# Kernel optimization log

Hardware: AMD Instinct MI355X
Metric: run time of the kernel (lower is better)

The kernel has to match this reference:

```python
import jax, jax.numpy as jnp
import numpy as np

NF = 64
UP = 4
# ktype 's' tap offsets within the 3x3 window
TAPS = ((0, 0), (0, 1), (1, 0), (1, 1))


def setup_inputs() -> dict:
    key = jax.random.key(0)
    ks = jax.random.split(key, 14)
    B, C, H, W = 8, 3, 192, 192
    x = jax.random.normal(ks[0], (B, C, H, W), dtype=jnp.float32)
    def lin(k, fan_in, fan_out):
        s = 1.0 / np.sqrt(fan_in)
        return jax.random.uniform(k, (fan_out, fan_in), jnp.float32, -s, s)
    def bias(k, fan_in, fan_out):
        s = 1.0 / np.sqrt(fan_in)
        return jax.random.uniform(k, (fan_out,), jnp.float32, -s, s)
    inp = {"x": x}
    inp["W1"], inp["b1"] = lin(ks[1], 4, NF), bias(ks[2], 4, NF)
    inp["W2"], inp["b2"] = lin(ks[3], NF, NF), bias(ks[4], NF, NF)
    inp["W3"], inp["b3"] = lin(ks[5], NF, NF), bias(ks[6], NF, NF)
    inp["W4"], inp["b4"] = lin(ks[7], NF, NF), bias(ks[8], NF, NF)
    inp["W5"], inp["b5"] = lin(ks[9], NF, NF), bias(ks[10], NF, NF)
    inp["W6"], inp["b6"] = lin(ks[11], NF, UP * UP), bias(ks[12], NF, UP * UP)
    return inp


def _forward(x, W1, b1, W2, b2, W3, b3, W4, b4, W5, b5, W6, b6):
    B, C, H, W = x.shape
    h, w = H - 2, W - 2
    xi = x.reshape(B * C, H, W)  # each channel processed independently
    taps = jnp.stack([xi[:, di:di + h, dj:dj + w] for di, dj in TAPS], axis=-1)
    # conv1: tiny 4->nf linear, then the outer act() in forward
    f = jax.nn.relu(jnp.einsum('nhwk,fk->nhwf', taps, W1) + b1)
    # conv2..conv5: 1x1 ActConv (conv then ReLU)
    for Wm, bm in ((W2, b2), (W3, b3), (W4, b4), (W5, b5)):
        f = jax.nn.relu(jnp.einsum('nhwf,gf->nhwg', f, Wm) + bm)
    # conv6: 1x1 to upscale^2 channels (no act)
    y = jnp.einsum('nhwf,gf->nhwg', f, W6) + b6  # [N, h, w, r*r]
    # pixel shuffle: out[h*r+i, w*r+j] = y[h, w, i*r+j]
    r = UP
    N = B * C
    y = y.reshape(N, h, w, r, r).transpose(0, 1, 3, 2, 4).reshape(N, h * r, w * r)
    return jnp.tanh(y).reshape(B, C, h * r, w * r)


def reference(x, W1, b1, W2, b2, W3, b3, W4, b4, W5, b5, W6, b6):
    return _forward(x, W1, b1, W2, b2, W3, b3, W4, b4, W5, b5, W6, b6)
```

## Files before the change

kernel.cpp:

```cpp
#include <hip/hip_runtime.h>
#include <cmath>


static constexpr int Hh = 190, Ww = 190, Him = 192, Wim = 192, Nimg = 24;
static constexpr int NPIX = Nimg * Hh * Ww;
static constexpr int NWG  = (NPIX + 511) / 512;

typedef __attribute__((ext_vector_type(8)))  _Float16 half8v;
typedef __attribute__((ext_vector_type(16))) float f32x16;
typedef __attribute__((ext_vector_type(4)))  unsigned int uint4v;

static constexpr int FR_L1  = 0;
static constexpr int FR_L6  = 2;
static constexpr int FR_MID = 6;
static constexpr int BT_BASE = 9728;

__global__ __launch_bounds__(256) void prep_kernel(
    const float* __restrict__ W1, const float* __restrict__ W2,
    const float* __restrict__ W3, const float* __restrict__ W4,
    const float* __restrict__ W5, const float* __restrict__ W6,
    const float* __restrict__ b1, const float* __restrict__ b2,
    const float* __restrict__ b3, const float* __restrict__ b4,
    const float* __restrict__ b5, const float* __restrict__ b6,
    short* __restrict__ ws) {
  float* wsF = (float*)ws;
  int t0 = blockIdx.x * 256 + threadIdx.x;
  int stride = gridDim.x * 256;
  for (int idx = t0; idx < 32 * 512; idx += stride) {
    int j = idx & 7, lane = (idx >> 3) & 63, fi = idx >> 9;
    int ks = fi & 3, mt = (fi >> 2) & 1, L = fi >> 3;
    const float* W = (L == 0) ? W2 : (L == 1) ? W3 : (L == 2) ? W4 : W5;
    int g = mt * 32 + (lane & 31);
    int k = (j & 3) + 8 * (2 * ks + (j >> 2)) + 4 * (lane >> 5);
    _Float16 h = (_Float16)W[g * 64 + k];
    ws[(FR_MID + fi) * 512 + (idx & 511)] = __builtin_bit_cast(short, h);
  }
  for (int idx = t0; idx < 2 * 512; idx += stride) {
    int j = idx & 7, lane = (idx >> 3) & 63, mt = idx >> 9;
    int g = mt * 32 + (lane & 31);
    float w = (j < 4) ? W1[g * 4 + j] : 0.f;
    _Float16 h = (_Float16)w;
    ws[(FR_L1 + mt) * 512 + (idx & 511)] = __builtin_bit_cast(short, h);
  }
  for (int idx = t0; idx < 4 * 512; idx += stride) {
    int j = idx & 7, lane = (idx >> 3) & 63, ks = idx >> 9;
    int g = lane & 31;
    int k = (j & 3) + 8 * (2 * ks + (j >> 2)) + 4 * (lane >> 5);
    float w = (g < 16) ? W6[g * 64 + k] : 0.f;
    _Float16 h = (_Float16)w;
    ws[(FR_L6 + ks) * 512 + (idx & 511)] = __builtin_bit_cast(short, h);
  }
  for (int idx = t0; idx < 256; idx += stride) {
    int r = idx & 15, b5v = (idx >> 4) & 1, mt = (idx >> 5) & 1, L = idx >> 6;
    const float* bb = (L == 0) ? b2 : (L == 1) ? b3 : (L == 2) ? b4 : b5;
    wsF[BT_BASE + idx] = bb[mt * 32 + (r >> 2) * 8 + b5v * 4 + (r & 3)];
  }
  for (int idx = t0; idx < 64; idx += stride) {
    int r = idx & 15, b5v = (idx >> 4) & 1, mt = idx >> 5;
    wsF[BT_BASE + 256 + idx] = b1[mt * 32 + (r >> 2) * 8 + b5v * 4 + (r & 3)];
  }
  for (int idx = t0; idx < 32; idx += stride) {
    int r = idx & 15, b5v = idx >> 4;
    wsF[BT_BASE + 320 + idx] = (r < 8) ? b6[(r >> 2) * 8 + b5v * 4 + (r & 3)] : 0.f;
  }
}


__device__ __forceinline__ unsigned pkrtz(float a, float b) {
  unsigned r;
  asm("v_cvt_pkrtz_f16_f32 %0, %1, %2" : "=v"(r) : "v"(a), "v"(b));
  return r;
}

__device__ __forceinline__ half8v mkfrag(unsigned a0, unsigned a1,
                                         unsigned b0, unsigned b1) {
  uint4v u = {a0, a1, b0, b1};
  return __builtin_bit_cast(half8v, u);
}

__device__ __forceinline__ void epilogue(f32x16 (&acc)[2][2],
    half8v (&f)[2][2][2]) {
#pragma unroll
  for (int mt = 0; mt < 2; ++mt)
#pragma unroll
    for (int nt = 0; nt < 2; ++nt)
#pragma unroll
      for (int s = 0; s < 2; ++s) {
        unsigned h[4];
#pragma unroll
        for (int d = 0; d < 4; ++d) {
          float v0 = fmaxf(acc[mt][nt][8 * s + 2 * d + 0], 0.f);
          float v1 = fmaxf(acc[mt][nt][8 * s + 2 * d + 1], 0.f);
          h[d] = pkrtz(v0, v1);
        }
        f[mt][nt][s] = mkfrag(h[0], h[1], h[2], h[3]);
      }
}

__device__ __forceinline__ void mid_layer(const short* wlds, const float* bt,
    int Lbase, int lane, int b5, half8v (&f)[2][2][2]) {
  f32x16 acc[2][2];
#pragma unroll
  for (int mt = 0; mt < 2; ++mt) {
    f32x16 bf = *(const f32x16*)(bt + (mt * 2 + b5) * 16);
    half8v a0 = *(const half8v*)(wlds + (Lbase + mt * 4) * 512 + lane * 8);
#pragma unroll
    for (int nt = 0; nt < 2; ++nt)
      acc[mt][nt] = __builtin_amdgcn_mfma_f32_32x32x16_f16(a0, f[0][nt][0], bf, 0, 0, 0);
  }
#pragma unroll
  for (int ks = 1; ks < 4; ++ks) {
#pragma unroll
    for (int mt = 0; mt < 2; ++mt) {
      half8v a = *(const half8v*)(wlds + (Lbase + mt * 4 + ks) * 512 + lane * 8);
      acc[mt][0] = __builtin_amdgcn_mfma_f32_32x32x16_f16(a, f[ks >> 1][0][ks & 1], acc[mt][0], 0, 0, 0);
      acc[mt][1] = __builtin_amdgcn_mfma_f32_32x32x16_f16(a, f[ks >> 1][1][ks & 1], acc[mt][1], 0, 0, 0);
    }
  }
  epilogue(acc, f);
}

__device__ __forceinline__ float ftanh(float x) {
  float e = __expf(2.0f * x);
  return 1.0f - __fdividef(2.0f, e + 1.0f);
}

__global__ __launch_bounds__(512, 4) void fused_kernel(
    const float* __restrict__ x, const short* __restrict__ ws,
    float* __restrict__ out) {
  __shared__ __align__(16) short wlds[16384];
  __shared__ __align__(16) short wl16[3072];
  __shared__ __align__(64) float blds[352];
  {
    int tid = threadIdx.x;
    const uint4v* src = (const uint4v*)ws;
    if (tid < 384) ((uint4v*)wl16)[tid] = src[tid];
    uint4v* dstM = (uint4v*)wlds;
#pragma unroll
    for (int it = 0; it < 4; ++it)
      dstM[it * 512 + tid] = src[384 + it * 512 + tid];
    const float* wsF = (const float*)ws;
    if (tid < 352) blds[tid] = wsF[BT_BASE + tid];
  }
  __syncthreads();

  const int lane = threadIdx.x & 63;
  const int wave = threadIdx.x >> 6;
  const int b5 = lane >> 5, lo5 = lane & 31;
  const int wavebase = blockIdx.x * 512 + wave * 64;

  half8v f[2][2][2];

  {
    int p = wavebase + lane;
    int pc = p < NPIX ? p : NPIX - 1;
    unsigned jj = (unsigned)pc % 190u;
    unsigned r  = (unsigned)pc / 190u;
    unsigned ii = r % 190u, nn = r / 190u;
    const float* xp = x + ((nn * 192u + ii) * 192u + jj);
    float t0 = xp[0], t1 = xp[1], t2 = xp[192], t3 = xp[193];
    unsigned th0 = pkrtz(t0, t1), th1 = pkrtz(t2, t3);
    unsigned z = 0u;
    unsigned s0h0 = (b5 == 0) ? th0 : z, s0h1 = (b5 == 0) ? th1 : z;
    unsigned s1h0 = (b5 == 1) ? th0 : z, s1h1 = (b5 == 1) ? th1 : z;
    half8v B0 = mkfrag(s0h0, s0h1, s0h0, s0h1);
    half8v B1 = mkfrag(s1h0, s1h1, s1h0, s1h1);
    f32x16 acc[2][2];
#pragma unroll
    for (int mt = 0; mt < 2; ++mt) {
      f32x16 bf = *(const f32x16*)(blds + 256 + (mt * 2 + b5) * 16);
      half8v a = *(const half8v*)(wl16 + (FR_L1 + mt) * 512 + lane * 8);
      acc[mt][0] = __builtin_amdgcn_mfma_f32_32x32x16_f16(a, B0, bf, 0, 0, 0);
      acc[mt][1] = __builtin_amdgcn_mfma_f32_32x32x16_f16(a, B1, bf, 0, 0, 0);
    }
    epilogue(acc, f);
  }

  mid_layer(wlds, blds + 0 * 64,  0,  lane, b5, f);
  mid_layer(wlds, blds + 1 * 64,  8,  lane, b5, f);
  mid_layer(wlds, blds + 2 * 64,  16, lane, b5, f);
  mid_layer(wlds, blds + 3 * 64,  24, lane, b5, f);

  {
    f32x16 c6 = *(const f32x16*)(blds + 320 + b5 * 16);
    f32x16 a6[2];
    {
      half8v a = *(const half8v*)(wl16 + (FR_L6 + 0) * 512 + lane * 8);
#pragma unroll
      for (int nt = 0; nt < 2; ++nt)
        a6[nt] = __builtin_amdgcn_mfma_f32_32x32x16_f16(a, f[0][nt][0], c6, 0, 0, 0);
    }
#pragma unroll
    for (int ks = 1; ks < 4; ++ks) {
      half8v a = *(const half8v*)(wl16 + (FR_L6 + ks) * 512 + lane * 8);
      a6[0] = __builtin_amdgcn_mfma_f32_32x32x16_f16(a, f[ks >> 1][0][ks & 1], a6[0], 0, 0, 0);
      a6[1] = __builtin_amdgcn_mfma_f32_32x32x16_f16(a, f[ks >> 1][1][ks & 1], a6[1], 0, 0, 0);
    }
#pragma unroll
    for (int nt = 0; nt < 2; ++nt) {
      int p2 = wavebase + nt * 32 + lo5;
      if (p2 < NPIX) {
        unsigned jj = (unsigned)p2 % 190u;
        unsigned r  = (unsigned)p2 / 190u;
        unsigned ii = r % 190u, nn = r / 190u;
        int base = (int)((nn * 760u + ii * 4u) * 760u + jj * 4u);
        float4 s0, s1;
        s0.x = ftanh(a6[nt][0]); s0.y = ftanh(a6[nt][1]);
        s0.z = ftanh(a6[nt][2]); s0.w = ftanh(a6[nt][3]);
        s1.x = ftanh(a6[nt][4]); s1.y = ftanh(a6[nt][5]);
        s1.z = ftanh(a6[nt][6]); s1.w = ftanh(a6[nt][7]);
        *reinterpret_cast<float4*>(out + base + b5 * 760) = s0;
        *reinterpret_cast<float4*>(out + base + (2 + b5) * 760) = s1;
      }
    }
  }
}

extern "C" void kernel_launch(void* const* d_in, const int* in_sizes, int n_in,
                              void* d_out, int out_size, void* d_ws, size_t ws_size,
                              hipStream_t stream) {
  const float* x  = (const float*)d_in[0];
  const float* W1 = (const float*)d_in[1];
  const float* b1 = (const float*)d_in[2];
  const float* W2 = (const float*)d_in[3];
  const float* b2 = (const float*)d_in[4];
  const float* W3 = (const float*)d_in[5];
  const float* b3 = (const float*)d_in[6];
  const float* W4 = (const float*)d_in[7];
  const float* b4 = (const float*)d_in[8];
  const float* W5 = (const float*)d_in[9];
  const float* b5 = (const float*)d_in[10];
  const float* W6 = (const float*)d_in[11];
  const float* b6 = (const float*)d_in[12];

  hipLaunchKernelGGL(prep_kernel, dim3(64), dim3(256), 0, stream,
                     W1, W2, W3, W4, W5, W6, b1, b2, b3, b4, b5, b6, (short*)d_ws);
  hipLaunchKernelGGL(fused_kernel, dim3(NWG), dim3(512), 0, stream,
                     x, (const short*)d_ws, (float*)d_out);
}
```

Before: 50.93 us.

## Ping-pong activation buffers per tile and hoist input loads before weight staging

Each MFMA tile's four K-steps now run back to back and the ReLU/pack epilogue follows right after. Activations are double-buffered (fA/fB) so the next layer's fragments are written while the previous ones are still being read. This needs only one live 16-float accumulator instead of four, which lowers register pressure and lets epilogue work overlap later MFMAs. The per-pixel input loads are also issued before the LDS weight staging and barrier, so global latency overlaps the weight copy. The cost is a serial dependency chain within each tile and two activation buffers that are live together.

```diff
diff --git a/kernel.cpp b/kernel.cpp
--- a/kernel.cpp
+++ b/kernel.cpp
@@ -78,46 +78,41 @@
   return __builtin_bit_cast(half8v, u);
 }
 
-__device__ __forceinline__ void epilogue(f32x16 (&acc)[2][2],
-    half8v (&f)[2][2][2]) {
-#pragma unroll
-  for (int mt = 0; mt < 2; ++mt)
-#pragma unroll
-    for (int nt = 0; nt < 2; ++nt)
-#pragma unroll
-      for (int s = 0; s < 2; ++s) {
-        unsigned h[4];
-#pragma unroll
-        for (int d = 0; d < 4; ++d) {
-          float v0 = fmaxf(acc[mt][nt][8 * s + 2 * d + 0], 0.f);
-          float v1 = fmaxf(acc[mt][nt][8 * s + 2 * d + 1], 0.f);
-          h[d] = pkrtz(v0, v1);
-        }
-        f[mt][nt][s] = mkfrag(h[0], h[1], h[2], h[3]);
-      }
+__device__ __forceinline__ void epi_tile(const f32x16& acc, half8v (&o)[2]) {
+#pragma unroll
+  for (int s = 0; s < 2; ++s) {
+    unsigned h[4];
+#pragma unroll
+    for (int d = 0; d < 4; ++d) {
+      float v0 = fmaxf(acc[8 * s + 2 * d + 0], 0.f);
+      float v1 = fmaxf(acc[8 * s + 2 * d + 1], 0.f);
+      h[d] = pkrtz(v0, v1);
+    }
+    o[s] = mkfrag(h[0], h[1], h[2], h[3]);
+  }
 }
 
 __device__ __forceinline__ void mid_layer(const short* wlds, const float* bt,
-    int Lbase, int lane, int b5, half8v (&f)[2][2][2]) {
-  f32x16 acc[2][2];
+    int Lbase, int lane, int b5,
+    half8v (&fo)[2][2][2], half8v (&fn)[2][2][2]) {
 #pragma unroll
   for (int mt = 0; mt < 2; ++mt) {
+    const short* wb = wlds + (Lbase + mt * 4) * 512 + lane * 8;
+    half8v a0 = *(const half8v*)(wb + 0 * 512);
+    half8v a1 = *(const half8v*)(wb + 1 * 512);
+    half8v a2 = *(const half8v*)(wb + 2 * 512);
+    half8v a3 = *(const half8v*)(wb + 3 * 512);
     f32x16 bf = *(const f32x16*)(bt + (mt * 2 + b5) * 16);
-    half8v a0 = *(const half8v*)(wlds + (Lbase + mt * 4) * 512 + lane * 8);
-#pragma unroll
-    for (int nt = 0; nt < 2; ++nt)
-      acc[mt][nt] = __builtin_amdgcn_mfma_f32_32x32x16_f16(a0, f[0][nt][0], bf, 0, 0, 0);
-  }
-#pragma unroll
-  for (int ks = 1; ks < 4; ++ks) {
-#pragma unroll
-    for (int mt = 0; mt < 2; ++mt) {
-      half8v a = *(const half8v*)(wlds + (Lbase + mt * 4 + ks) * 512 + lane * 8);
-      acc[mt][0] = __builtin_amdgcn_mfma_f32_32x32x16_f16(a, f[ks >> 1][0][ks & 1], acc[mt][0], 0, 0, 0);
-      acc[mt][1] = __builtin_amdgcn_mfma_f32_32x32x16_f16(a, f[ks >> 1][1][ks & 1], acc[mt][1], 0, 0, 0);
-    }
-  }
-  epilogue(acc, f);
+#pragma unroll
+    for (int nt = 0; nt < 2; ++nt) {
+      f32x16 acc;
+      acc = __builtin_amdgcn_mfma_f32_32x32x16_f16(a0, fo[0][nt][0], bf, 0, 0, 0);
+      acc = __builtin_amdgcn_mfma_f32_32x32x16_f16(a1, fo[0][nt][1], acc, 0, 0, 0);
+      acc = __builtin_amdgcn_mfma_f32_32x32x16_f16(a2, fo[1][nt][0], acc, 0, 0, 0);
+      acc = __builtin_amdgcn_mfma_f32_32x32x16_f16(a3, fo[1][nt][1], acc, 0, 0, 0);
+      epi_tile(acc, fn[mt][nt]);
+    }
+  }
 }
 
 __device__ __forceinline__ float ftanh(float x) {
@@ -131,6 +126,20 @@
   __shared__ __align__(16) short wlds[16384];
   __shared__ __align__(16) short wl16[3072];
   __shared__ __align__(64) float blds[352];
+
+  const int lane = threadIdx.x & 63;
+  const int wave = threadIdx.x >> 6;
+  const int b5 = lane >> 5, lo5 = lane & 31;
+  const int wavebase = blockIdx.x * 512 + wave * 64;
+
+  int p = wavebase + lane;
+  int pc = p < NPIX ? p : NPIX - 1;
+  unsigned jj0 = (unsigned)pc % 190u;
+  unsigned r0  = (unsigned)pc / 190u;
+  unsigned ii0 = r0 % 190u, nn0 = r0 / 190u;
+  const float* xp = x + ((nn0 * 192u + ii0) * 192u + jj0);
+  float t0 = xp[0], t1 = xp[1], t2 = xp[192], t3 = xp[193];
+
   {
     int tid = threadIdx.x;
     const uint4v* src = (const uint4v*)ws;
@@ -144,60 +153,47 @@
   }
   __syncthreads();
 
-  const int lane = threadIdx.x & 63;
-  const int wave = threadIdx.x >> 6;
-  const int b5 = lane >> 5, lo5 = lane & 31;
-  const int wavebase = blockIdx.x * 512 + wave * 64;
-
-  half8v f[2][2][2];
+  half8v fA[2][2][2], fB[2][2][2];
 
   {
-    int p = wavebase + lane;
-    int pc = p < NPIX ? p : NPIX - 1;
-    unsigned jj = (unsigned)pc % 190u;
-    unsigned r  = (unsigned)pc / 190u;
-    unsigned ii = r % 190u, nn = r / 190u;
-    const float* xp = x + ((nn * 192u + ii) * 192u + jj);
-    float t0 = xp[0], t1 = xp[1], t2 = xp[192], t3 = xp[193];
     unsigned th0 = pkrtz(t0, t1), th1 = pkrtz(t2, t3);
     unsigned z = 0u;
     unsigned s0h0 = (b5 == 0) ? th0 : z, s0h1 = (b5 == 0) ? th1 : z;
     unsigned s1h0 = (b5 == 1) ? th0 : z, s1h1 = (b5 == 1) ? th1 : z;
-    half8v B0 = mkfrag(s0h0, s0h1, s0h0, s0h1);
-    half8v B1 = mkfrag(s1h0, s1h1, s1h0, s1h1);
-    f32x16 acc[2][2];
+    half8v Bv[2];
+    Bv[0] = mkfrag(s0h0, s0h1, s0h0, s0h1);
+    Bv[1] = mkfrag(s1h0, s1h1, s1h0, s1h1);
 #pragma unroll
     for (int mt = 0; mt < 2; ++mt) {
       f32x16 bf = *(const f32x16*)(blds + 256 + (mt * 2 + b5) * 16);
       half8v a = *(const half8v*)(wl16 + (FR_L1 + mt) * 512 + lane * 8);
-      acc[mt][0] = __builtin_amdgcn_mfma_f32_32x32x16_f16(a, B0, bf, 0, 0, 0);
-      acc[mt][1] = __builtin_amdgcn_mfma_f32_32x32x16_f16(a, B1, bf, 0, 0, 0);
-    }
-    epilogue(acc, f);
-  }
-
-  mid_layer(wlds, blds + 0 * 64,  0,  lane, b5, f);
-  mid_layer(wlds, blds + 1 * 64,  8,  lane, b5, f);
-  mid_layer(wlds, blds + 2 * 64,  16, lane, b5, f);
-  mid_layer(wlds, blds + 3 * 64,  24, lane, b5, f);
+#pragma unroll
+      for (int nt = 0; nt < 2; ++nt) {
+        f32x16 acc = __builtin_amdgcn_mfma_f32_32x32x16_f16(a, Bv[nt], bf, 0, 0, 0);
+        epi_tile(acc, fA[mt][nt]);
+      }
+    }
+  }
+
+  mid_layer(wlds, blds + 0 * 64, 0,  lane, b5, fA, fB);
+  mid_layer(wlds, blds + 1 * 64, 8,  lane, b5, fB, fA);
+  mid_layer(wlds, blds + 2 * 64, 16, lane, b5, fA, fB);
+  mid_layer(wlds, blds + 3 * 64, 24, lane, b5, fB, fA);
 
   {
     f32x16 c6 = *(const f32x16*)(blds + 320 + b5 * 16);
-    f32x16 a6[2];
-    {
-      half8v a = *(const half8v*)(wl16 + (FR_L6 + 0) * 512 + lane * 8);
-#pragma unroll
-      for (int nt = 0; nt < 2; ++nt)
-        a6[nt] = __builtin_amdgcn_mfma_f32_32x32x16_f16(a, f[0][nt][0], c6, 0, 0, 0);
-    }
-#pragma unroll
-    for (int ks = 1; ks < 4; ++ks) {
-      half8v a = *(const half8v*)(wl16 + (FR_L6 + ks) * 512 + lane * 8);
-      a6[0] = __builtin_amdgcn_mfma_f32_32x32x16_f16(a, f[ks >> 1][0][ks & 1], a6[0], 0, 0, 0);
-      a6[1] = __builtin_amdgcn_mfma_f32_32x32x16_f16(a, f[ks >> 1][1][ks & 1], a6[1], 0, 0, 0);
-    }
+    const short* wb = wl16 + FR_L6 * 512 + lane * 8;
+    half8v a0 = *(const half8v*)(wb + 0 * 512);
+    half8v a1 = *(const half8v*)(wb + 1 * 512);
+    half8v a2 = *(const half8v*)(wb + 2 * 512);
+    half8v a3 = *(const half8v*)(wb + 3 * 512);
 #pragma unroll
     for (int nt = 0; nt < 2; ++nt) {
+      f32x16 a6;
+      a6 = __builtin_amdgcn_mfma_f32_32x32x16_f16(a0, fA[0][nt][0], c6, 0, 0, 0);
+      a6 = __builtin_amdgcn_mfma_f32_32x32x16_f16(a1, fA[0][nt][1], a6, 0, 0, 0);
+      a6 = __builtin_amdgcn_mfma_f32_32x32x16_f16(a2, fA[1][nt][0], a6, 0, 0, 0);
+      a6 = __builtin_amdgcn_mfma_f32_32x32x16_f16(a3, fA[1][nt][1], a6, 0, 0, 0);
       int p2 = wavebase + nt * 32 + lo5;
       if (p2 < NPIX) {
         unsigned jj = (unsigned)p2 % 190u;
@@ -205,10 +201,10 @@
         unsigned ii = r % 190u, nn = r / 190u;
         int base = (int)((nn * 760u + ii * 4u) * 760u + jj * 4u);
         float4 s0, s1;
-        s0.x = ftanh(a6[nt][0]); s0.y = ftanh(a6[nt][1]);
-        s0.z = ftanh(a6[nt][2]); s0.w = ftanh(a6[nt][3]);
-        s1.x = ftanh(a6[nt][4]); s1.y = ftanh(a6[nt][5]);
-        s1.z = ftanh(a6[nt][6]); s1.w = ftanh(a6[nt][7]);
+        s0.x = ftanh(a6[0]); s0.y = ftanh(a6[1]);
+        s0.z = ftanh(a6[2]); s0.w = ftanh(a6[3]);
+        s1.x = ftanh(a6[4]); s1.y = ftanh(a6[5]);
+        s1.z = ftanh(a6[6]); s1.w = ftanh(a6[7]);
         *reinterpret_cast<float4*>(out + base + b5 * 760) = s0;
         *reinterpret_cast<float4*>(out + base + (2 + b5) * 760) = s1;
       }
```

Result: no change. 50.39 us, median of 2 (-1.1%).
